# Kernel tuning notes

Measured on AMD Instinct MI355X. Metric: run time of the kernel, lower is better.

## Reference

```python
import jax, jax.numpy as jnp
import numpy as np

B, S, D, H = 2, 2048, 1024, 16
HD = D // H  # 64
LN_EPS = 1e-5


def setup_inputs() -> dict:
    key = jax.random.key(0)
    ks = jax.random.split(key, 5)
    hidden_states = jax.random.normal(ks[0], (B, S, D), dtype=jnp.float32)
    attention_mask = jnp.zeros((B, 1, 1, S), dtype=jnp.float32)  # additive mask
    # LayerNorm params
    ln_gamma = jnp.ones((D,), dtype=jnp.float32)
    ln_beta = jnp.zeros((D,), dtype=jnp.float32)
    # Q/K/V projections, no bias; stored as [in, out]
    sc = 1.0 / np.sqrt(D)
    Wq = jax.random.normal(ks[1], (D, D), dtype=jnp.float32) * sc
    Wk = jax.random.normal(ks[2], (D, D), dtype=jnp.float32) * sc
    Wv = jax.random.normal(ks[3], (D, D), dtype=jnp.float32) * sc
    return {"hidden_states": hidden_states, "attention_mask": attention_mask,
            "ln_gamma": ln_gamma, "ln_beta": ln_beta, "Wq": Wq, "Wk": Wk, "Wv": Wv}


def _layernorm(x, g, b):
    mu = jnp.mean(x, axis=-1, keepdims=True)
    var = jnp.mean(jnp.square(x - mu), axis=-1, keepdims=True)
    return (x - mu) * jax.lax.rsqrt(var + LN_EPS) * g + b


def reference(hidden_states, attention_mask, ln_gamma, ln_beta, Wq, Wk, Wv):
    h = _layernorm(hidden_states, ln_gamma, ln_beta)          # [B,S,D]
    # project and split heads: [B,S,D] -> [B,H,S,HD]
    def split_heads(x):
        return x.reshape(B, S, H, HD).transpose(0, 2, 1, 3)
    q = split_heads(h @ Wq)
    k = split_heads(h @ Wk)
    v = split_heads(h @ Wv)
    scores = jnp.einsum('bhqd,bhkd->bhqk', q, k) / jnp.sqrt(jnp.float32(HD))
    scores = scores + attention_mask                           # additive mask broadcast
    probs = jax.nn.softmax(scores, axis=-1)                    # dropout p=0 -> identity
    ctx = jnp.einsum('bhqk,bhkd->bhqd', probs, v)              # [B,H,S,HD]
    ctx = ctx.transpose(0, 2, 1, 3).reshape(B, S, H * HD)      # [B,S,D]
    return ctx
```

## Files before the change

kernel.cpp:

```cpp
#include <hip/hip_runtime.h>
#include <hip/hip_bf16.h>
#include <cstdint>

#define B_ 2
#define S_ 2048
#define D_ 1024
#define H_ 16
#define HD_ 64
#define M_ (B_*S_)

#define LOG2E 1.4426950408889634f
#define C1_ (0.125f * LOG2E)

typedef unsigned short u16;
typedef __bf16 bf16x8 __attribute__((ext_vector_type(8)));
typedef u16 u16x8 __attribute__((ext_vector_type(8)));
typedef float f32x4 __attribute__((ext_vector_type(4)));
typedef float f32x16 __attribute__((ext_vector_type(16)));
typedef int i32x4 __attribute__((ext_vector_type(4)));

static __device__ __forceinline__ u16 f2bu(float f) {
  __bf16 b = (__bf16)f;
  return __builtin_bit_cast(unsigned short, b);
}

static __device__ __forceinline__ int cvtpk(float a, float b) {
  int r;
  asm("v_cvt_pk_bf16_f32 %0, %1, %2" : "=v"(r) : "v"(a), "v"(b));
  return r;
}
static __device__ __forceinline__ void plswap(int &x, int &y) {
  asm("v_permlane32_swap_b32 %0, %1" : "+v"(x), "+v"(y));
}

#define GLOAD16(g, l) __builtin_amdgcn_global_load_lds( \
    (__attribute__((address_space(1))) void*)(g), \
    (__attribute__((address_space(3))) void*)(l), 16, 0, 0)

__global__ __launch_bounds__(256) void ln_kernel(const float* __restrict__ x,
    const float* __restrict__ g, const float* __restrict__ be, u16* __restrict__ h) {
  const int row = blockIdx.x;
  const int t = threadIdx.x;
  float4 v = reinterpret_cast<const float4*>(x + (size_t)row * D_)[t];
  float s = v.x + v.y + v.z + v.w;
  float sq = v.x*v.x + v.y*v.y + v.z*v.z + v.w*v.w;
  #pragma unroll
  for (int off = 32; off >= 1; off >>= 1) {
    s  += __shfl_down(s, off);
    sq += __shfl_down(sq, off);
  }
  __shared__ float red[8];
  const int wave = t >> 6, lane = t & 63;
  if (lane == 0) { red[wave] = s; red[4 + wave] = sq; }
  __syncthreads();
  if (t == 0) {
    float ts = red[0]+red[1]+red[2]+red[3];
    float tq = red[4]+red[5]+red[6]+red[7];
    float mu = ts * (1.0f / D_);
    red[0] = mu;
    red[1] = rsqrtf(tq * (1.0f / D_) - mu*mu + 1e-5f);
  }
  __syncthreads();
  const float mu = red[0], rs = red[1];
  float4 gg = reinterpret_cast<const float4*>(g)[t];
  float4 bb = reinterpret_cast<const float4*>(be)[t];
  ushort4 o;
  o.x = f2bu((v.x - mu) * rs * gg.x + bb.x);
  o.y = f2bu((v.y - mu) * rs * gg.y + bb.y);
  o.z = f2bu((v.z - mu) * rs * gg.z + bb.z);
  o.w = f2bu((v.w - mu) * rs * gg.w + bb.w);
  reinterpret_cast<ushort4*>(h + (size_t)row * D_)[t] = o;
}

__global__ __launch_bounds__(256) void wt_kernel(const float* __restrict__ W0,
    const float* __restrict__ W1, const float* __restrict__ W2, u16* __restrict__ wt) {
  const int z = blockIdx.z;
  const float* W = (z == 0) ? W0 : ((z == 1) ? W1 : W2);
  u16* out = wt + (size_t)z * D_ * D_;
  __shared__ float tile[32][33];
  const int n0 = blockIdx.x * 32, k0 = blockIdx.y * 32;
  const int tx = threadIdx.x, ty = threadIdx.y;
  #pragma unroll
  for (int j = 0; j < 4; ++j)
    tile[ty + 8*j][tx] = W[(size_t)(k0 + ty + 8*j) * D_ + n0 + tx];
  __syncthreads();
  #pragma unroll
  for (int j = 0; j < 4; ++j)
    out[(size_t)(n0 + ty + 8*j) * D_ + k0 + tx] = f2bu(tile[tx][ty + 8*j]);
}

__global__ __launch_bounds__(256) void qkv_gemm(const u16* __restrict__ hbuf,
    const u16* __restrict__ wt, u16* __restrict__ qkv) {
  const int z = blockIdx.z;
  const u16* Bt = wt + (size_t)z * D_ * D_;
  u16* outp = qkv + (size_t)z * (B_*H_*S_*HD_);
  __shared__ __align__(16) u16 As[128 * 32];
  __shared__ __align__(16) u16 Bs[128 * 32];
  const int t = threadIdx.x, lane = t & 63, wave = t >> 6;
  const int row0 = blockIdx.y * 128, col0 = blockIdx.x * 128;
  const int wm = wave >> 1, wn = wave & 1;
  f32x4 acc[4][4] = {};
  const u16* ag = hbuf + (size_t)(row0 + (t >> 2)) * D_ + (t & 3) * 8;
  const u16* bg = Bt   + (size_t)(col0 + (t >> 2)) * D_ + (t & 3) * 8;
  u16* lA = &As[wave * 512];
  u16* lB = &Bs[wave * 512];

  for (int k0 = 0; k0 < D_; k0 += 32) {
    GLOAD16(ag + k0,           lA);
    GLOAD16(ag + k0 + 64 * D_, lA + 2048);
    GLOAD16(bg + k0,           lB);
    GLOAD16(bg + k0 + 64 * D_, lB + 2048);
    __syncthreads();
    bf16x8 af[4], bfr[4];
    #pragma unroll
    for (int m = 0; m < 4; ++m)
      af[m] = *reinterpret_cast<const bf16x8*>(&As[(wm*64 + m*16 + (lane & 15)) * 32 + (lane >> 4) * 8]);
    #pragma unroll
    for (int n = 0; n < 4; ++n)
      bfr[n] = *reinterpret_cast<const bf16x8*>(&Bs[(wn*64 + n*16 + (lane & 15)) * 32 + (lane >> 4) * 8]);
    #pragma unroll
    for (int m = 0; m < 4; ++m) {
      #pragma unroll
      for (int n = 0; n < 4; ++n)
        acc[m][n] = __builtin_amdgcn_mfma_f32_16x16x32_bf16(af[m], bfr[n], acc[m][n], 0, 0, 0);
    }
    __syncthreads();
  }
  #pragma unroll
  for (int m = 0; m < 4; ++m) {
    #pragma unroll
    for (int n = 0; n < 4; ++n) {
      const int gcol = col0 + wn*64 + n*16 + (lane & 15);
      const int hI = gcol >> 6, dI = gcol & 63;
      #pragma unroll
      for (int r = 0; r < 4; ++r) {
        const int grow = row0 + wm*64 + m*16 + (lane >> 4) * 4 + r;
        const int bI = grow >> 11, sI = grow & (S_ - 1);
        size_t idx;
        if (z == 2) idx = ((size_t)(bI * H_ + hI) * HD_ + dI) * S_ + sI;
        else        idx = ((size_t)(bI * H_ + hI) * S_ + sI) * HD_ + dI;
        outp[idx] = f2bu(acc[m][n][r]);
      }
    }
  }
}

__global__ __launch_bounds__(512) void attn_kernel(const u16* __restrict__ qkv,
    const float* __restrict__ mask, float* __restrict__ out) {
  const int bid = blockIdx.x;
  const int qt = (bid >> 3) & 7;
  const int pidx = (bid & 7) + ((bid >> 6) << 3);
  const int hI = pidx & 15, bI = pidx >> 4;
  const size_t plane = (size_t)pidx * (S_ * HD_);
  const u16* Qp  = qkv + plane;
  const u16* Kp  = qkv + (size_t)(B_*H_*S_*HD_) + plane;
  const u16* Vtp = qkv + 2*(size_t)(B_*H_*S_*HD_) + plane;

  const int t = threadIdx.x, lane = t & 63, wave = t >> 6;
  const int cl = lane & 31, hf = lane >> 5;

  __shared__ __align__(16) u16 KsBuf[2][64 * 64];
  __shared__ __align__(16) u16 VsBuf[2][64 * 64];
  __shared__ float maskLds[S_];

  {
    float4 mv = reinterpret_cast<const float4*>(mask + (size_t)bI * S_)[t];
    float4 sm = {mv.x * LOG2E, mv.y * LOG2E, mv.z * LOG2E, mv.w * LOG2E};
    reinterpret_cast<float4*>(maskLds)[t] = sm;
  }

  const int q0 = qt * 256 + wave * 32;
  bf16x8 qf[4];
  #pragma unroll
  for (int dstep = 0; dstep < 4; ++dstep)
    qf[dstep] = *reinterpret_cast<const bf16x8*>(
        Qp + (size_t)(q0 + cl) * HD_ + dstep * 16 + hf * 8);

  const int sr = t >> 3;
  const int scb = (t & 7) * 16;
  const int scol = (scb ^ ((sr & 7) << 4)) >> 1;
  const u16* kSrcBase = Kp  + (size_t)sr * HD_ + scol;
  const u16* vSrcBase = Vtp + (size_t)sr * S_  + scol;

  f32x16 oacc0 = {}, oacc1 = {};
  float m = -1e30f, lsum = 0.f;

  GLOAD16(kSrcBase, &KsBuf[0][wave * 512]);
  GLOAD16(vSrcBase, &VsBuf[0][wave * 512]);
  int cur = 0;

  for (int kv0 = 0; kv0 < S_; kv0 += 64) {
    __syncthreads();
    if (kv0 + 64 < S_) {
      GLOAD16(kSrcBase + (size_t)(kv0 + 64) * HD_, &KsBuf[cur ^ 1][wave * 512]);
      GLOAD16(vSrcBase + (kv0 + 64),               &VsBuf[cur ^ 1][wave * 512]);
    }
    const char* Ks = (const char*)KsBuf[cur];
    const char* Vs = (const char*)VsBuf[cur];

    #pragma unroll
    for (int sub = 0; sub < 2; ++sub) {
      f32x16 sacc = {};
      const int krow = sub * 32 + cl;
      const int kswz = (krow & 7) << 4;
      #pragma unroll
      for (int dstep = 0; dstep < 4; ++dstep) {
        bf16x8 kf = *reinterpret_cast<const bf16x8*>(
            Ks + krow * 128 + ((dstep * 32 + hf * 16) ^ kswz));
        sacc = __builtin_amdgcn_mfma_f32_32x32x16_bf16(kf, qf[dstep], sacc, 0, 0, 0);
      }
      const int kvb = kv0 + sub * 32;
      float4 m0 = *reinterpret_cast<const float4*>(&maskLds[kvb + 4 * hf]);
      float4 m1 = *reinterpret_cast<const float4*>(&maskLds[kvb + 8 + 4 * hf]);
      float4 m2 = *reinterpret_cast<const float4*>(&maskLds[kvb + 16 + 4 * hf]);
      float4 m3 = *reinterpret_cast<const float4*>(&maskLds[kvb + 24 + 4 * hf]);
      float z[16];
      #pragma unroll
      for (int r = 0; r < 4; ++r) {
        z[r]      = sacc[r]      * C1_ + ((const float*)&m0)[r];
        z[r + 4]  = sacc[r + 4]  * C1_ + ((const float*)&m1)[r];
        z[r + 8]  = sacc[r + 8]  * C1_ + ((const float*)&m2)[r];
        z[r + 12] = sacc[r + 12] * C1_ + ((const float*)&m3)[r];
      }
      float tm = z[0];
      #pragma unroll
      for (int r = 1; r < 16; ++r) tm = fmaxf(tm, z[r]);
      tm = fmaxf(tm, __shfl_xor(tm, 32));
      const float mnew = fmaxf(m, tm);
      const float sf = __builtin_amdgcn_exp2f(m - mnew);
      m = mnew;
      float p[16]; float rs = 0.f;
      #pragma unroll
      for (int r = 0; r < 16; ++r) { p[r] = __builtin_amdgcn_exp2f(z[r] - mnew); rs += p[r]; }
      rs += __shfl_xor(rs, 32);
      lsum = lsum * sf + rs;
      oacc0 = oacc0 * sf;
      oacc1 = oacc1 * sf;
      int pk01 = cvtpk(p[0], p[1]),  pk23 = cvtpk(p[2], p[3]);
      int pk45 = cvtpk(p[4], p[5]),  pk67 = cvtpk(p[6], p[7]);
      int pk89 = cvtpk(p[8], p[9]),  pkAB = cvtpk(p[10], p[11]);
      int pkCD = cvtpk(p[12], p[13]), pkEF = cvtpk(p[14], p[15]);
      plswap(pk01, pk45);
      plswap(pk23, pk67);
      plswap(pk89, pkCD);
      plswap(pkAB, pkEF);
      i32x4 c0 = {pk01, pk23, pk45, pk67};
      i32x4 c1 = {pk89, pkAB, pkCD, pkEF};
      bf16x8 pf0 = __builtin_bit_cast(bf16x8, c0);
      bf16x8 pf1 = __builtin_bit_cast(bf16x8, c1);
      const int vrow0 = cl, vrow1 = 32 + cl;
      const int vswz0 = (vrow0 & 7) << 4, vswz1 = (vrow1 & 7) << 4;
      const int kb0 = (sub * 32 + hf * 8) * 2;
      const int kb1 = (sub * 32 + 16 + hf * 8) * 2;
      bf16x8 vf;
      vf = *reinterpret_cast<const bf16x8*>(Vs + vrow0 * 128 + (kb0 ^ vswz0));
      oacc0 = __builtin_amdgcn_mfma_f32_32x32x16_bf16(vf, pf0, oacc0, 0, 0, 0);
      vf = *reinterpret_cast<const bf16x8*>(Vs + vrow1 * 128 + (kb0 ^ vswz1));
      oacc1 = __builtin_amdgcn_mfma_f32_32x32x16_bf16(vf, pf0, oacc1, 0, 0, 0);
      vf = *reinterpret_cast<const bf16x8*>(Vs + vrow0 * 128 + (kb1 ^ vswz0));
      oacc0 = __builtin_amdgcn_mfma_f32_32x32x16_bf16(vf, pf1, oacc0, 0, 0, 0);
      vf = *reinterpret_cast<const bf16x8*>(Vs + vrow1 * 128 + (kb1 ^ vswz1));
      oacc1 = __builtin_amdgcn_mfma_f32_32x32x16_bf16(vf, pf1, oacc1, 0, 0, 0);
    }
    cur ^= 1;
  }

  const float rinv = 1.0f / lsum;
  float* orow = out + ((size_t)bI * S_ + q0 + cl) * D_ + hI * HD_;
  #pragma unroll
  for (int j = 0; j < 4; ++j) {
    float4 o0 = {oacc0[4*j] * rinv, oacc0[4*j+1] * rinv, oacc0[4*j+2] * rinv, oacc0[4*j+3] * rinv};
    float4 o1 = {oacc1[4*j] * rinv, oacc1[4*j+1] * rinv, oacc1[4*j+2] * rinv, oacc1[4*j+3] * rinv};
    *reinterpret_cast<float4*>(orow + 8*j + 4*hf)      = o0;
    *reinterpret_cast<float4*>(orow + 32 + 8*j + 4*hf) = o1;
  }
}

extern "C" void kernel_launch(void* const* d_in, const int* in_sizes, int n_in,
                              void* d_out, int out_size, void* d_ws, size_t ws_size,
                              hipStream_t stream) {
  const float* x     = (const float*)d_in[0];
  const float* mask  = (const float*)d_in[1];
  const float* gamma = (const float*)d_in[2];
  const float* beta  = (const float*)d_in[3];
  const float* Wq    = (const float*)d_in[4];
  const float* Wk    = (const float*)d_in[5];
  const float* Wv    = (const float*)d_in[6];
  float* out = (float*)d_out;

  char* ws = (char*)d_ws;
  u16* hbuf = (u16*)ws;
  u16* wt   = (u16*)(ws + (size_t)M_*D_*2);
  u16* qkv  = (u16*)(ws + (size_t)M_*D_*2 + 3ull*D_*D_*2);

  hipLaunchKernelGGL(ln_kernel, dim3(M_), dim3(256), 0, stream, x, gamma, beta, hbuf);
  hipLaunchKernelGGL(wt_kernel, dim3(32, 32, 3), dim3(32, 8), 0, stream, Wq, Wk, Wv, wt);
  hipLaunchKernelGGL(qkv_gemm, dim3(8, 32, 3), dim3(256), 0, stream, hbuf, wt, qkv);
  hipLaunchKernelGGL(attn_kernel, dim3(256), dim3(512), 0, stream, qkv, mask, out);
}
```

Before: 113.6 us.

## Swizzle GEMM LDS, lazy softmax rescale, smaller attention blocks with priority hints

The QKV GEMM now XOR-swizzles its LDS chunk layout to cut bank conflicts on fragment reads. The attention kernel moves to 256-thread blocks (4 waves, 128 query rows) with a 512-block grid and two blocks per CU, and each wave now loads two rows per K/V tile. Softmax gets a lazy-rescale scheme: the running max only updates when it is exceeded by more than 8 (log2 domain), and the mask is pre-offset by -8, so most iterations skip rescaling the accumulators. s_setprio hints are placed around MFMA sections to interleave matrix and softmax work across waves. The threshold trick trades some headroom in exp range for fewer rescales.

```diff
diff --git a/kernel.cpp b/kernel.cpp
--- a/kernel.cpp
+++ b/kernel.cpp
@@ -100,10 +100,14 @@
   const int row0 = blockIdx.y * 128, col0 = blockIdx.x * 128;
   const int wm = wave >> 1, wn = wave & 1;
   f32x4 acc[4][4] = {};
-  const u16* ag = hbuf + (size_t)(row0 + (t >> 2)) * D_ + (t & 3) * 8;
-  const u16* bg = Bt   + (size_t)(col0 + (t >> 2)) * D_ + (t & 3) * 8;
+  const int schunk = (t & 3) ^ ((t >> 3) & 3);
+  const u16* ag = hbuf + (size_t)(row0 + (t >> 2)) * D_ + schunk * 8;
+  const u16* bg = Bt   + (size_t)(col0 + (t >> 2)) * D_ + schunk * 8;
   u16* lA = &As[wave * 512];
   u16* lB = &Bs[wave * 512];
+  const char* Ac = (const char*)As;
+  const char* Bc = (const char*)Bs;
+  const int cbase = (((lane >> 4) ^ ((lane >> 1) & 3)) << 4);
 
   for (int k0 = 0; k0 < D_; k0 += 32) {
     GLOAD16(ag + k0,           lA);
@@ -114,10 +118,10 @@
     bf16x8 af[4], bfr[4];
     #pragma unroll
     for (int m = 0; m < 4; ++m)
-      af[m] = *reinterpret_cast<const bf16x8*>(&As[(wm*64 + m*16 + (lane & 15)) * 32 + (lane >> 4) * 8]);
+      af[m] = *reinterpret_cast<const bf16x8*>(Ac + (wm*64 + m*16 + (lane & 15)) * 64 + cbase);
     #pragma unroll
     for (int n = 0; n < 4; ++n)
-      bfr[n] = *reinterpret_cast<const bf16x8*>(&Bs[(wn*64 + n*16 + (lane & 15)) * 32 + (lane >> 4) * 8]);
+      bfr[n] = *reinterpret_cast<const bf16x8*>(Bc + (wn*64 + n*16 + (lane & 15)) * 64 + cbase);
     #pragma unroll
     for (int m = 0; m < 4; ++m) {
       #pragma unroll
@@ -145,11 +149,62 @@
   }
 }
 
-__global__ __launch_bounds__(512) void attn_kernel(const u16* __restrict__ qkv,
+static __device__ __forceinline__ void sm_pack(
+    const f32x16& s, const float* __restrict__ mrow, int hf,
+    float& dm, float& lsum, f32x16& o0, f32x16& o1,
+    bf16x8& pfA, bf16x8& pfB) {
+  float4 m0 = *reinterpret_cast<const float4*>(mrow + 4*hf);
+  float4 m1 = *reinterpret_cast<const float4*>(mrow + 8 + 4*hf);
+  float4 m2 = *reinterpret_cast<const float4*>(mrow + 16 + 4*hf);
+  float4 m3 = *reinterpret_cast<const float4*>(mrow + 24 + 4*hf);
+  float zb[16];
+  #pragma unroll
+  for (int r = 0; r < 4; ++r) {
+    zb[r]      = s[r]      * C1_ + ((const float*)&m0)[r];
+    zb[r + 4]  = s[r + 4]  * C1_ + ((const float*)&m1)[r];
+    zb[r + 8]  = s[r + 8]  * C1_ + ((const float*)&m2)[r];
+    zb[r + 12] = s[r + 12] * C1_ + ((const float*)&m3)[r];
+  }
+  float a0 = fmaxf(fmaxf(zb[0], zb[1]), zb[2]);
+  float a1 = fmaxf(fmaxf(zb[3], zb[4]), zb[5]);
+  float a2 = fmaxf(fmaxf(zb[6], zb[7]), zb[8]);
+  float a3 = fmaxf(fmaxf(zb[9], zb[10]), zb[11]);
+  float a4 = fmaxf(fmaxf(zb[12], zb[13]), zb[14]);
+  float tm = fmaxf(fmaxf(fmaxf(a0, a1), fmaxf(a2, a3)), fmaxf(a4, zb[15]));
+  tm = fmaxf(tm, __shfl_xor(tm, 32));
+  if (__builtin_expect(__any(tm > dm + 8.0f), 0)) {
+    float dnew = fmaxf(dm, tm - 8.0f);
+    float sf = __builtin_amdgcn_exp2f(dm - dnew);
+    lsum *= sf; o0 = o0 * sf; o1 = o1 * sf; dm = dnew;
+  }
+  float p[16];
+  #pragma unroll
+  for (int r = 0; r < 16; ++r) p[r] = __builtin_amdgcn_exp2f(zb[r] - dm);
+  float s01 = (p[0] + p[1]) + (p[2] + p[3]);
+  float s23 = (p[4] + p[5]) + (p[6] + p[7]);
+  float s45 = (p[8] + p[9]) + (p[10] + p[11]);
+  float s67 = (p[12] + p[13]) + (p[14] + p[15]);
+  float rs = (s01 + s23) + (s45 + s67);
+  rs += __shfl_xor(rs, 32);
+  lsum += rs;
+  int pk01 = cvtpk(p[0], p[1]),   pk23 = cvtpk(p[2], p[3]);
+  int pk45 = cvtpk(p[4], p[5]),   pk67 = cvtpk(p[6], p[7]);
+  int pk89 = cvtpk(p[8], p[9]),   pkAB = cvtpk(p[10], p[11]);
+  int pkCD = cvtpk(p[12], p[13]), pkEF = cvtpk(p[14], p[15]);
+  plswap(pk01, pk45); plswap(pk23, pk67);
+  plswap(pk89, pkCD); plswap(pkAB, pkEF);
+  i32x4 c0 = {pk01, pk23, pk45, pk67};
+  i32x4 c1 = {pk89, pkAB, pkCD, pkEF};
+  pfA = __builtin_bit_cast(bf16x8, c0);
+  pfB = __builtin_bit_cast(bf16x8, c1);
+}
+
+__global__ __launch_bounds__(256, 2) void attn_kernel(const u16* __restrict__ qkv,
     const float* __restrict__ mask, float* __restrict__ out) {
   const int bid = blockIdx.x;
-  const int qt = (bid >> 3) & 7;
-  const int pidx = (bid & 7) + ((bid >> 6) << 3);
+  const int x = bid & 7, rr = bid >> 3;
+  const int j = rr & 15;
+  const int pidx = x + ((rr >> 4) << 3);
   const int hI = pidx & 15, bI = pidx >> 4;
   const size_t plane = (size_t)pidx * (S_ * HD_);
   const u16* Qp  = qkv + plane;
@@ -158,121 +213,111 @@
 
   const int t = threadIdx.x, lane = t & 63, wave = t >> 6;
   const int cl = lane & 31, hf = lane >> 5;
+  const int swz = (cl & 7) << 4;
 
   __shared__ __align__(16) u16 KsBuf[2][64 * 64];
   __shared__ __align__(16) u16 VsBuf[2][64 * 64];
   __shared__ float maskLds[S_];
 
-  {
-    float4 mv = reinterpret_cast<const float4*>(mask + (size_t)bI * S_)[t];
-    float4 sm = {mv.x * LOG2E, mv.y * LOG2E, mv.z * LOG2E, mv.w * LOG2E};
-    reinterpret_cast<float4*>(maskLds)[t] = sm;
-  }
-
-  const int q0 = qt * 256 + wave * 32;
+  #pragma unroll
+  for (int i = 0; i < 2; ++i) {
+    float4 mv = reinterpret_cast<const float4*>(mask + (size_t)bI * S_)[t + i*256];
+    float4 sm = {mv.x * LOG2E - 8.0f, mv.y * LOG2E - 8.0f,
+                 mv.z * LOG2E - 8.0f, mv.w * LOG2E - 8.0f};
+    reinterpret_cast<float4*>(maskLds)[t + i*256] = sm;
+  }
+
+  const int q0 = j * 128 + wave * 32;
   bf16x8 qf[4];
   #pragma unroll
-  for (int dstep = 0; dstep < 4; ++dstep)
-    qf[dstep] = *reinterpret_cast<const bf16x8*>(
-        Qp + (size_t)(q0 + cl) * HD_ + dstep * 16 + hf * 8);
+  for (int d = 0; d < 4; ++d)
+    qf[d] = *reinterpret_cast<const bf16x8*>(
+        Qp + (size_t)(q0 + cl) * HD_ + d * 16 + hf * 8);
 
   const int sr = t >> 3;
-  const int scb = (t & 7) * 16;
-  const int scol = (scb ^ ((sr & 7) << 4)) >> 1;
-  const u16* kSrcBase = Kp  + (size_t)sr * HD_ + scol;
-  const u16* vSrcBase = Vtp + (size_t)sr * S_  + scol;
+  const int scol = (((t & 7) * 16) ^ ((sr & 7) << 4)) >> 1;
+  const u16* kSrc = Kp  + (size_t)sr * HD_ + scol;
+  const u16* vSrc = Vtp + (size_t)sr * S_  + scol;
+  const int L0 = wave * 512, L1 = 2048 + wave * 512;
 
   f32x16 oacc0 = {}, oacc1 = {};
-  float m = -1e30f, lsum = 0.f;
-
-  GLOAD16(kSrcBase, &KsBuf[0][wave * 512]);
-  GLOAD16(vSrcBase, &VsBuf[0][wave * 512]);
+  float dm = 0.f, lsum = 0.f;
+
+  GLOAD16(kSrc,                  &KsBuf[0][L0]);
+  GLOAD16(kSrc + 32 * HD_,       &KsBuf[0][L1]);
+  GLOAD16(vSrc,                  &VsBuf[0][L0]);
+  GLOAD16(vSrc + 32 * (size_t)S_, &VsBuf[0][L1]);
   int cur = 0;
 
   for (int kv0 = 0; kv0 < S_; kv0 += 64) {
     __syncthreads();
     if (kv0 + 64 < S_) {
-      GLOAD16(kSrcBase + (size_t)(kv0 + 64) * HD_, &KsBuf[cur ^ 1][wave * 512]);
-      GLOAD16(vSrcBase + (kv0 + 64),               &VsBuf[cur ^ 1][wave * 512]);
+      const u16* kn = kSrc + (size_t)(kv0 + 64) * HD_;
+      const u16* vn = vSrc + (kv0 + 64);
+      GLOAD16(kn,                   &KsBuf[cur ^ 1][L0]);
+      GLOAD16(kn + 32 * HD_,        &KsBuf[cur ^ 1][L1]);
+      GLOAD16(vn,                   &VsBuf[cur ^ 1][L0]);
+      GLOAD16(vn + 32 * (size_t)S_, &VsBuf[cur ^ 1][L1]);
     }
     const char* Ks = (const char*)KsBuf[cur];
     const char* Vs = (const char*)VsBuf[cur];
 
-    #pragma unroll
-    for (int sub = 0; sub < 2; ++sub) {
-      f32x16 sacc = {};
-      const int krow = sub * 32 + cl;
-      const int kswz = (krow & 7) << 4;
-      #pragma unroll
-      for (int dstep = 0; dstep < 4; ++dstep) {
-        bf16x8 kf = *reinterpret_cast<const bf16x8*>(
-            Ks + krow * 128 + ((dstep * 32 + hf * 16) ^ kswz));
-        sacc = __builtin_amdgcn_mfma_f32_32x32x16_bf16(kf, qf[dstep], sacc, 0, 0, 0);
-      }
-      const int kvb = kv0 + sub * 32;
-      float4 m0 = *reinterpret_cast<const float4*>(&maskLds[kvb + 4 * hf]);
-      float4 m1 = *reinterpret_cast<const float4*>(&maskLds[kvb + 8 + 4 * hf]);
-      float4 m2 = *reinterpret_cast<const float4*>(&maskLds[kvb + 16 + 4 * hf]);
-      float4 m3 = *reinterpret_cast<const float4*>(&maskLds[kvb + 24 + 4 * hf]);
-      float z[16];
-      #pragma unroll
-      for (int r = 0; r < 4; ++r) {
-        z[r]      = sacc[r]      * C1_ + ((const float*)&m0)[r];
-        z[r + 4]  = sacc[r + 4]  * C1_ + ((const float*)&m1)[r];
-        z[r + 8]  = sacc[r + 8]  * C1_ + ((const float*)&m2)[r];
-        z[r + 12] = sacc[r + 12] * C1_ + ((const float*)&m3)[r];
-      }
-      float tm = z[0];
-      #pragma unroll
-      for (int r = 1; r < 16; ++r) tm = fmaxf(tm, z[r]);
-      tm = fmaxf(tm, __shfl_xor(tm, 32));
-      const float mnew = fmaxf(m, tm);
-      const float sf = __builtin_amdgcn_exp2f(m - mnew);
-      m = mnew;
-      float p[16]; float rs = 0.f;
-      #pragma unroll
-      for (int r = 0; r < 16; ++r) { p[r] = __builtin_amdgcn_exp2f(z[r] - mnew); rs += p[r]; }
-      rs += __shfl_xor(rs, 32);
-      lsum = lsum * sf + rs;
-      oacc0 = oacc0 * sf;
-      oacc1 = oacc1 * sf;
-      int pk01 = cvtpk(p[0], p[1]),  pk23 = cvtpk(p[2], p[3]);
-      int pk45 = cvtpk(p[4], p[5]),  pk67 = cvtpk(p[6], p[7]);
-      int pk89 = cvtpk(p[8], p[9]),  pkAB = cvtpk(p[10], p[11]);
-      int pkCD = cvtpk(p[12], p[13]), pkEF = cvtpk(p[14], p[15]);
-      plswap(pk01, pk45);
-      plswap(pk23, pk67);
-      plswap(pk89, pkCD);
-      plswap(pkAB, pkEF);
-      i32x4 c0 = {pk01, pk23, pk45, pk67};
-      i32x4 c1 = {pk89, pkAB, pkCD, pkEF};
-      bf16x8 pf0 = __builtin_bit_cast(bf16x8, c0);
-      bf16x8 pf1 = __builtin_bit_cast(bf16x8, c1);
-      const int vrow0 = cl, vrow1 = 32 + cl;
-      const int vswz0 = (vrow0 & 7) << 4, vswz1 = (vrow1 & 7) << 4;
-      const int kb0 = (sub * 32 + hf * 8) * 2;
-      const int kb1 = (sub * 32 + 16 + hf * 8) * 2;
+    f32x16 s0 = {}, s1 = {};
+    __builtin_amdgcn_s_setprio(1);
+    #pragma unroll
+    for (int d = 0; d < 4; ++d) {
+      bf16x8 kf = *reinterpret_cast<const bf16x8*>(
+          Ks + cl * 128 + ((d * 32 + hf * 16) ^ swz));
+      s0 = __builtin_amdgcn_mfma_f32_32x32x16_bf16(kf, qf[d], s0, 0, 0, 0);
+    }
+    #pragma unroll
+    for (int d = 0; d < 4; ++d) {
+      bf16x8 kf = *reinterpret_cast<const bf16x8*>(
+          Ks + (32 + cl) * 128 + ((d * 32 + hf * 16) ^ swz));
+      s1 = __builtin_amdgcn_mfma_f32_32x32x16_bf16(kf, qf[d], s1, 0, 0, 0);
+    }
+    __builtin_amdgcn_s_setprio(0);
+
+    bf16x8 pA, pB;
+    sm_pack(s0, maskLds + kv0, hf, dm, lsum, oacc0, oacc1, pA, pB);
+    __builtin_amdgcn_s_setprio(1);
+    {
       bf16x8 vf;
-      vf = *reinterpret_cast<const bf16x8*>(Vs + vrow0 * 128 + (kb0 ^ vswz0));
-      oacc0 = __builtin_amdgcn_mfma_f32_32x32x16_bf16(vf, pf0, oacc0, 0, 0, 0);
-      vf = *reinterpret_cast<const bf16x8*>(Vs + vrow1 * 128 + (kb0 ^ vswz1));
-      oacc1 = __builtin_amdgcn_mfma_f32_32x32x16_bf16(vf, pf0, oacc1, 0, 0, 0);
-      vf = *reinterpret_cast<const bf16x8*>(Vs + vrow0 * 128 + (kb1 ^ vswz0));
-      oacc0 = __builtin_amdgcn_mfma_f32_32x32x16_bf16(vf, pf1, oacc0, 0, 0, 0);
-      vf = *reinterpret_cast<const bf16x8*>(Vs + vrow1 * 128 + (kb1 ^ vswz1));
-      oacc1 = __builtin_amdgcn_mfma_f32_32x32x16_bf16(vf, pf1, oacc1, 0, 0, 0);
-    }
+      vf = *reinterpret_cast<const bf16x8*>(Vs + cl * 128 + ((hf * 16) ^ swz));
+      oacc0 = __builtin_amdgcn_mfma_f32_32x32x16_bf16(vf, pA, oacc0, 0, 0, 0);
+      vf = *reinterpret_cast<const bf16x8*>(Vs + (32 + cl) * 128 + ((hf * 16) ^ swz));
+      oacc1 = __builtin_amdgcn_mfma_f32_32x32x16_bf16(vf, pA, oacc1, 0, 0, 0);
+      vf = *reinterpret_cast<const bf16x8*>(Vs + cl * 128 + ((32 + hf * 16) ^ swz));
+      oacc0 = __builtin_amdgcn_mfma_f32_32x32x16_bf16(vf, pB, oacc0, 0, 0, 0);
+      vf = *reinterpret_cast<const bf16x8*>(Vs + (32 + cl) * 128 + ((32 + hf * 16) ^ swz));
+      oacc1 = __builtin_amdgcn_mfma_f32_32x32x16_bf16(vf, pB, oacc1, 0, 0, 0);
+    }
+    __builtin_amdgcn_s_setprio(0);
+    sm_pack(s1, maskLds + kv0 + 32, hf, dm, lsum, oacc0, oacc1, pA, pB);
+    __builtin_amdgcn_s_setprio(1);
+    {
+      bf16x8 vf;
+      vf = *reinterpret_cast<const bf16x8*>(Vs + cl * 128 + ((64 + hf * 16) ^ swz));
+      oacc0 = __builtin_amdgcn_mfma_f32_32x32x16_bf16(vf, pA, oacc0, 0, 0, 0);
+      vf = *reinterpret_cast<const bf16x8*>(Vs + (32 + cl) * 128 + ((64 + hf * 16) ^ swz));
+      oacc1 = __builtin_amdgcn_mfma_f32_32x32x16_bf16(vf, pA, oacc1, 0, 0, 0);
+      vf = *reinterpret_cast<const bf16x8*>(Vs + cl * 128 + ((96 + hf * 16) ^ swz));
+      oacc0 = __builtin_amdgcn_mfma_f32_32x32x16_bf16(vf, pB, oacc0, 0, 0, 0);
+      vf = *reinterpret_cast<const bf16x8*>(Vs + (32 + cl) * 128 + ((96 + hf * 16) ^ swz));
+      oacc1 = __builtin_amdgcn_mfma_f32_32x32x16_bf16(vf, pB, oacc1, 0, 0, 0);
+    }
+    __builtin_amdgcn_s_setprio(0);
     cur ^= 1;
   }
 
   const float rinv = 1.0f / lsum;
   float* orow = out + ((size_t)bI * S_ + q0 + cl) * D_ + hI * HD_;
   #pragma unroll
-  for (int j = 0; j < 4; ++j) {
-    float4 o0 = {oacc0[4*j] * rinv, oacc0[4*j+1] * rinv, oacc0[4*j+2] * rinv, oacc0[4*j+3] * rinv};
-    float4 o1 = {oacc1[4*j] * rinv, oacc1[4*j+1] * rinv, oacc1[4*j+2] * rinv, oacc1[4*j+3] * rinv};
-    *reinterpret_cast<float4*>(orow + 8*j + 4*hf)      = o0;
-    *reinterpret_cast<float4*>(orow + 32 + 8*j + 4*hf) = o1;
+  for (int jj = 0; jj < 4; ++jj) {
+    float4 o0 = {oacc0[4*jj] * rinv, oacc0[4*jj+1] * rinv, oacc0[4*jj+2] * rinv, oacc0[4*jj+3] * rinv};
+    float4 o1 = {oacc1[4*jj] * rinv, oacc1[4*jj+1] * rinv, oacc1[4*jj+2] * rinv, oacc1[4*jj+3] * rinv};
+    *reinterpret_cast<float4*>(orow + 8*jj + 4*hf)      = o0;
+    *reinterpret_cast<float4*>(orow + 32 + 8*jj + 4*hf) = o1;
   }
 }
 
@@ -296,5 +341,5 @@
   hipLaunchKernelGGL(ln_kernel, dim3(M_), dim3(256), 0, stream, x, gamma, beta, hbuf);
   hipLaunchKernelGGL(wt_kernel, dim3(32, 32, 3), dim3(32, 8), 0, stream, Wq, Wk, Wv, wt);
   hipLaunchKernelGGL(qkv_gemm, dim3(8, 32, 3), dim3(256), 0, stream, hbuf, wt, qkv);
-  hipLaunchKernelGGL(attn_kernel, dim3(256), dim3(512), 0, stream, qkv, mask, out);
-}
+  hipLaunchKernelGGL(attn_kernel, dim3(512), dim3(256), 0, stream, qkv, mask, out);
+}
```

Measured after the change: 111.0 us. -2.3%, faster.
